# Kernel optimization log

Measured on AMD Instinct MI355X. Metric: run time of the kernel, lower is better.

## Reference

```python
import math
import jax, jax.numpy as jnp
import numpy as np

B, N, L, D, H = 1, 64, 512, 768, 12
DK = D // H


def setup_inputs() -> dict:
    rng = jax.random.key(0)
    ks = jax.random.split(rng, 8)
    s = 0.02  # weight init scale
    return {
        "query": jax.random.normal(ks[0], (B, N, L, D), jnp.float32),
        "key": jax.random.normal(ks[1], (B, N, L, D), jnp.float32),
        "value": jax.random.normal(ks[2], (B, N, L, D), jnp.float32),
        "Wq": jax.random.normal(ks[3], (D, D), jnp.float32) * s,
        "bq": jnp.zeros((D,), jnp.float32),
        "Wk": jax.random.normal(ks[4], (D, D), jnp.float32) * s,
        "bk": jnp.zeros((D,), jnp.float32),
        "Wv": jax.random.normal(ks[5], (D, D), jnp.float32) * s,
        "bv": jnp.zeros((D,), jnp.float32),
        "Wo": jax.random.normal(ks[6], (D, D), jnp.float32) * s,
        "bo": jnp.zeros((D,), jnp.float32),
    }


def reference(query, key, value, Wq, bq, Wk, bk, Wv, bv, Wo, bo):
    b, n, l, d = query.shape
    h, dk = H, DK
    # combined scaling: 1/sqrt(d_k) * 1/sqrt(N)
    scale = 1.0 / (math.sqrt(dk) * math.sqrt(n))
    # nn.Linear: y = x @ W.T + b  (W is [out, in])
    q = (jnp.einsum('bnld,ed->bnle', query, Wq) + bq).reshape(b, n, l, h, dk) * scale
    k = (jnp.einsum('bnld,ed->bnle', key, Wk) + bk).reshape(b, n, l, h, dk)
    v = (jnp.einsum('bnld,ed->bnle', value, Wv) + bv).reshape(b, n, l, h, dk)
    # tied attention: scores summed over the N (sequence-copy) axis BEFORE softmax
    att = jnp.einsum('bnihk,bnjhk->bhij', q, k)  # [B,H,L,L]
    att = jax.nn.softmax(att, axis=-1)  # dropout is identity in eval
    # single attention map broadcast across all N value tensors
    out = jnp.einsum('bhij,bnjhk->bnihk', att, v).reshape(b, n, l, d)
    return jnp.einsum('bnld,ed->bnle', out, Wo) + bo
```

## Files before the change

kernel.cpp:

```cpp
#include <hip/hip_runtime.h>


typedef __bf16 bf16x8 __attribute__((ext_vector_type(8)));
typedef float f32x4 __attribute__((ext_vector_type(4)));

__device__ __forceinline__ unsigned short f2bf(float f) {
  unsigned u = __float_as_uint(f);
  u += 0x7fffu + ((u >> 16) & 1u);
  return (unsigned short)(u >> 16);
}

__device__ __forceinline__ void gll16(const void* g, void* l) {
  __builtin_amdgcn_global_load_lds(
      (const __attribute__((address_space(1))) unsigned int*)g,
      (__attribute__((address_space(3))) unsigned int*)l, 16, 0, 0);
}

#define BAR __builtin_amdgcn_s_barrier()

enum { MODE_QCAT = 0, MODE_VT = 1, MODE_ATT = 2, MODE_OUTWS = 3, MODE_OUT_BIAS = 4 };

template <int MODE>
__global__ __launch_bounds__(512, 2) void gemm256(
    const void* __restrict__ Av, const void* __restrict__ Bv,
    const float* __restrict__ b0, const float* __restrict__ b1,
    void* __restrict__ Cv, int K, int lda, int ldb,
    long long a_bs, long long b_bs, float alpha0, float alpha1,
    long long c_bs, int ntn) {
  __shared__ unsigned short L[2][2][16384];

  const int tid = threadIdx.x;
  const int wave = tid >> 6;
  const int lane = tid & 63;
  const int wm = wave >> 2;
  const int wn = wave & 3;
  const int l15 = lane & 15;
  const int kq8 = lane >> 4;
  const int sw = l15 & 7;

  const int bid = blockIdx.x;
  const int xcd = bid & 7;
  const int kk_ = bid >> 3;
  const int tn = kk_ % ntn;
  const int tm = (kk_ / ntn) * 8 + xcd;
  const int batch = blockIdx.z;

  const long long m0 = (long long)tm * 256;
  const long long n0 = (long long)tn * 256;

  const unsigned short* Ab = (const unsigned short*)Av + (long long)batch * a_bs;
  const unsigned short* Bb = (const unsigned short*)Bv + (long long)batch * b_bs;

  const long long rowAw = m0 + wave * 8 + (lane >> 3);
  const long long rowBw = n0 + wave * 8 + (lane >> 3);
  const int csw = ((lane & 7) ^ (lane >> 3)) << 3;

  f32x4 acc[8][4] = {};

  auto stA = [&](int buf, int q, int k0) {
    gll16(Ab + (rowAw + (q << 6)) * (long long)lda + k0 + csw,
          &L[buf][0][(q << 12) + (wave << 9)]);
  };
  auto stB = [&](int buf, int q, int k0) {
    gll16(Bb + (rowBw + (q << 6)) * (long long)ldb + k0 + csw,
          &L[buf][1][(q << 12) + (wave << 9)]);
  };

  float bpre[4] = {};
  float aa = 1.0f;
  if constexpr (MODE == MODE_QCAT || MODE == MODE_VT || MODE == MODE_OUT_BIAS) {
    const float* bb = batch ? b1 : b0;
    aa = batch ? alpha1 : alpha0;
#pragma unroll
    for (int u = 0; u < 4; ++u) bpre[u] = bb[n0 + wn * 64 + u * 16 + l15];
  }

  const int NT = K >> 6;
#pragma unroll
  for (int q = 0; q < 4; ++q) stB(0, q, 0);
#pragma unroll
  for (int q = 0; q < 4; ++q) stA(0, q, 0);
  if (NT > 1) {
    stA(1, 0, 64);
    stA(1, 2, 64);
    asm volatile("s_waitcnt vmcnt(2)" ::: "memory");
  } else {
    asm volatile("s_waitcnt vmcnt(0)" ::: "memory");
  }
  BAR;

  for (int T = 0; T < NT; ++T) {
    const int cur = T & 1, nxt = cur ^ 1;
    const int k1 = (T + 1) << 6, k2 = (T + 2) << 6;
#pragma unroll
    for (int p = 0; p < 4; ++p) {
      const int kc = p >> 1, mh = p & 1;
      bf16x8 af[4], bfr[4];
#pragma unroll
      for (int mf = 0; mf < 4; ++mf) {
        const int row = wm * 128 + mh * 64 + mf * 16 + l15;
        af[mf] = *(const bf16x8*)&L[cur][0][row * 64 + (((kc << 2) + kq8) ^ sw) * 8];
      }
#pragma unroll
      for (int u = 0; u < 4; ++u) {
        const int row = wn * 64 + u * 16 + l15;
        bfr[u] = *(const bf16x8*)&L[cur][1][row * 64 + (((kc << 2) + kq8) ^ sw) * 8];
      }
      if (p == 0 && T + 1 < NT) { stB(nxt, 0, k1); stB(nxt, 1, k1); }
      if (p == 1 && T + 1 < NT) { stB(nxt, 2, k1); stB(nxt, 3, k1); }
      if (p == 2 && T + 1 < NT) { stA(nxt, 1, k1); stA(nxt, 3, k1); }
      if (p == 3 && T + 2 < NT) { stA(cur, 0, k2); stA(cur, 2, k2); }
      __builtin_amdgcn_s_setprio(1);
#pragma unroll
      for (int mf = 0; mf < 4; ++mf)
#pragma unroll
        for (int u = 0; u < 4; ++u)
          acc[mh * 4 + mf][u] = __builtin_amdgcn_mfma_f32_16x16x32_bf16(
              af[mf], bfr[u], acc[mh * 4 + mf][u], 0, 0, 0);
      __builtin_amdgcn_s_setprio(0);
      if (p == 3) {
        if (T + 1 < NT) {
          if (T + 2 < NT) asm volatile("s_waitcnt vmcnt(2)" ::: "memory");
          else            asm volatile("s_waitcnt vmcnt(0)" ::: "memory");
          BAR;
        }
      } else {
        BAR;
      }
    }
  }

#pragma unroll
  for (int mf = 0; mf < 8; ++mf) {
#pragma unroll
    for (int u = 0; u < 4; ++u) {
      const long long col = n0 + wn * 64 + u * 16 + l15;
#pragma unroll
      for (int r = 0; r < 4; ++r) {
        const long long row = m0 + wm * 128 + mf * 16 + (lane >> 4) * 4 + r;
        float v = acc[mf][u][r];
        if constexpr (MODE == MODE_QCAT) {
          const float vv = (v + bpre[u]) * aa;
          const long long h = col >> 6, kq = col & 63, n = row >> 9, i = row & 511;
          ((unsigned short*)Cv + batch * c_bs)[((h * 512 + i) << 12) + (n << 6) + kq] =
              f2bf(vv);
        } else if constexpr (MODE == MODE_VT) {
          const float vv = v + bpre[u];
          const long long h = col >> 6, kq = col & 63, n = row >> 9, j = row & 511;
          ((unsigned short*)Cv)[(((h << 12) + (n << 6) + kq) << 9) + j] = f2bf(vv);
        } else {
          ((float*)Cv)[row * 768 + col] = v + bpre[u];
        }
      }
    }
  }
}

constexpr int BM = 128, BN = 128, BK = 32;

template <int MODE, bool SWZ, int KS>
__global__ __launch_bounds__(256, 2) void gemm_bt(
    const void* __restrict__ Av, const void* __restrict__ Bv,
    const float* __restrict__ bias, void* __restrict__ Cv,
    int K, int lda, int ldb, long long a_bs, long long b_bs,
    float alpha, int ntn, long long c_bs) {
  constexpr int LP = 32;

  __shared__ unsigned short As0[BM * LP];
  __shared__ unsigned short Bs0[BN * LP];
  __shared__ unsigned short As1[BM * LP];
  __shared__ unsigned short Bs1[BN * LP];

  const int tid = threadIdx.x;
  const int wave = tid >> 6;
  const int lane = tid & 63;
  const int wm = wave >> 1, wn = wave & 1;

  int tm, tn, batch = 0, ks = 0;
  if constexpr (SWZ && MODE == MODE_ATT) {
    const int bid = blockIdx.x;
    const int xcd = bid & 7, j = bid >> 3;
    const int z = (j >> 4) * 8 + xcd;
    const int tile = j & 15;
    tn = tile & 3;
    tm = tile >> 2;
    ks = z % KS;
    batch = z / KS;
  } else if constexpr (SWZ && MODE == MODE_OUTWS) {
    const int bid = blockIdx.x;
    const int xcd = bid & 7, j = bid >> 3;
    const int g = (j >> 6) * 8 + xcd;
    const int idx = j & 63;
    batch = g >> 1;
    tm = idx >> 4;
    tn = (g & 1) * 16 + (idx & 15);
  } else {
    if constexpr (SWZ) {
      const int bid = blockIdx.x;
      const int xcd = bid & 7;
      const int k = bid >> 3;
      tn = k % ntn;
      tm = (k / ntn) * 8 + xcd;
    } else {
      tn = blockIdx.x;
      tm = blockIdx.y;
    }
    batch = blockIdx.z;
    if constexpr (KS > 1) { ks = batch % KS; batch /= KS; }
  }

  const long long m0 = (long long)tm * BM;
  const long long n0 = (long long)tn * BN;

  const unsigned short* Ab = (const unsigned short*)Av + (long long)batch * a_bs + (long long)ks * K;
  const unsigned short* Bb = (const unsigned short*)Bv + (long long)batch * b_bs + (long long)ks * K;

  f32x4 acc[4][4] = {};

  const int l15 = lane & 15;
  const int kq = (lane >> 4) * 8;
  const int r_in = lane >> 2;
  const int c8 = (lane & 3) * 8;

  auto stage = [&](unsigned short* Asb, unsigned short* Bsb, int k0) {
#pragma unroll
    for (int t = 0; t < 2; ++t) {
      const int rb = t * 64 + wave * 16;
      gll16(Ab + (m0 + rb + r_in) * (long long)lda + k0 + c8, &Asb[rb * LP]);
      gll16(Bb + (n0 + rb + r_in) * (long long)ldb + k0 + c8, &Bsb[rb * LP]);
    }
  };
  auto compute = [&](const unsigned short* Asb, const unsigned short* Bsb) {
    bf16x8 af[4], bfr[4];
#pragma unroll
    for (int t = 0; t < 4; ++t)
      af[t] = *(const bf16x8*)&Asb[(wm * 64 + t * 16 + l15) * LP + kq];
#pragma unroll
    for (int u = 0; u < 4; ++u)
      bfr[u] = *(const bf16x8*)&Bsb[(wn * 64 + u * 16 + l15) * LP + kq];
#pragma unroll
    for (int t = 0; t < 4; ++t)
#pragma unroll
      for (int u = 0; u < 4; ++u)
        acc[t][u] = __builtin_amdgcn_mfma_f32_16x16x32_bf16(af[t], bfr[u], acc[t][u], 0, 0, 0);
  };

  stage(As0, Bs0, 0);
  asm volatile("s_waitcnt vmcnt(0)" ::: "memory");
  BAR;

  const int NT = K >> 5;
  for (int t = 0; t < NT; t += 2) {
    stage(As1, Bs1, (t + 1) << 5);
    asm volatile("s_waitcnt vmcnt(4)" ::: "memory");
    BAR;
    compute(As0, Bs0);
    BAR;
    if (t + 2 < NT) {
      stage(As0, Bs0, (t + 2) << 5);
      asm volatile("s_waitcnt vmcnt(4)" ::: "memory");
    } else {
      asm volatile("s_waitcnt vmcnt(0)" ::: "memory");
    }
    BAR;
    compute(As1, Bs1);
    BAR;
  }

#pragma unroll
  for (int t = 0; t < 4; ++t) {
#pragma unroll
    for (int u = 0; u < 4; ++u) {
      const long long col = n0 + wn * 64 + u * 16 + l15;
#pragma unroll
      for (int r = 0; r < 4; ++r) {
        const long long row = m0 + wm * 64 + t * 16 + (lane >> 4) * 4 + r;
        float v = acc[t][u][r];
        if constexpr (MODE == MODE_ATT) {
          float* p = &((float*)Cv)[((long long)batch << 18) + (row << 9) + col];
          if constexpr (KS > 1) atomicAdd(p, v); else *p = v;
        } else if constexpr (MODE == MODE_OUTWS) {
          const long long n = col >> 6, kk = col & 63;
          ((unsigned short*)Cv)[(n * 512 + row) * 768 + (long long)batch * 64 + kk] = f2bf(v);
        } else {
          ((float*)Cv)[row * 768 + col] = v + alpha;
        }
      }
    }
  }
}

__global__ __launch_bounds__(256) void softmax_rows(const float* __restrict__ att,
                                                    unsigned short* __restrict__ outb) {
  const long long rowbase = (long long)blockIdx.x << 9;
  const int tid = threadIdx.x;
  float a = att[rowbase + tid];
  float b = att[rowbase + tid + 256];

  float m = fmaxf(a, b);
#pragma unroll
  for (int off = 32; off; off >>= 1) m = fmaxf(m, __shfl_down(m, off));
  __shared__ float redm[4];
  if ((tid & 63) == 0) redm[tid >> 6] = m;
  __syncthreads();
  m = fmaxf(fmaxf(redm[0], redm[1]), fmaxf(redm[2], redm[3]));

  const float e0 = __expf(a - m), e1 = __expf(b - m);
  float s = e0 + e1;
#pragma unroll
  for (int off = 32; off; off >>= 1) s += __shfl_down(s, off);
  __shared__ float reds[4];
  if ((tid & 63) == 0) reds[tid >> 6] = s;
  __syncthreads();
  s = reds[0] + reds[1] + reds[2] + reds[3];

  const float inv = 1.0f / s;
  outb[rowbase + tid] = f2bf(e0 * inv);
  outb[rowbase + tid + 256] = f2bf(e1 * inv);
}

__global__ __launch_bounds__(256) void cvt_bf16(const float* __restrict__ in,
                                                unsigned short* __restrict__ out) {
  const long long i = ((long long)blockIdx.x * 256 + threadIdx.x) * 8;
  const float4 a = *(const float4*)(in + i);
  const float4 b = *(const float4*)(in + i + 4);
  uint4 p;
  p.x = (unsigned)f2bf(a.x) | ((unsigned)f2bf(a.y) << 16);
  p.y = (unsigned)f2bf(a.z) | ((unsigned)f2bf(a.w) << 16);
  p.z = (unsigned)f2bf(b.x) | ((unsigned)f2bf(b.y) << 16);
  p.w = (unsigned)f2bf(b.z) | ((unsigned)f2bf(b.w) << 16);
  *(uint4*)(out + i) = p;
}

__global__ __launch_bounds__(256) void cvt_qk(
    const float* __restrict__ s0, const float* __restrict__ s1,
    unsigned short* __restrict__ d0, unsigned short* __restrict__ d1) {
  const float* s = blockIdx.y ? s1 : s0;
  unsigned short* d = blockIdx.y ? d1 : d0;
  const long long i = ((long long)blockIdx.x * 256 + threadIdx.x) * 8;
  const float4 a = *(const float4*)(s + i);
  const float4 b = *(const float4*)(s + i + 4);
  uint4 p;
  p.x = (unsigned)f2bf(a.x) | ((unsigned)f2bf(a.y) << 16);
  p.y = (unsigned)f2bf(a.z) | ((unsigned)f2bf(a.w) << 16);
  p.z = (unsigned)f2bf(b.x) | ((unsigned)f2bf(b.y) << 16);
  p.w = (unsigned)f2bf(b.z) | ((unsigned)f2bf(b.w) << 16);
  *(uint4*)(d + i) = p;
}

__global__ __launch_bounds__(256) void cvt_w4(
    const float* __restrict__ s0, const float* __restrict__ s1,
    const float* __restrict__ s2, const float* __restrict__ s3,
    unsigned short* __restrict__ d0, unsigned short* __restrict__ d1,
    unsigned short* __restrict__ d2, unsigned short* __restrict__ d3) {
  const float* s;
  unsigned short* d;
  switch (blockIdx.y) {
    case 0: s = s0; d = d0; break;
    case 1: s = s1; d = d1; break;
    case 2: s = s2; d = d2; break;
    default: s = s3; d = d3; break;
  }
  const long long i = ((long long)blockIdx.x * 256 + threadIdx.x) * 8;
  const float4 a = *(const float4*)(s + i);
  const float4 b = *(const float4*)(s + i + 4);
  uint4 p;
  p.x = (unsigned)f2bf(a.x) | ((unsigned)f2bf(a.y) << 16);
  p.y = (unsigned)f2bf(a.z) | ((unsigned)f2bf(a.w) << 16);
  p.z = (unsigned)f2bf(b.x) | ((unsigned)f2bf(b.y) << 16);
  p.w = (unsigned)f2bf(b.z) | ((unsigned)f2bf(b.w) << 16);
  *(uint4*)(d + i) = p;
}

extern "C" void kernel_launch(void* const* d_in, const int* in_sizes, int n_in,
                              void* d_out, int out_size, void* d_ws, size_t ws_size,
                              hipStream_t stream) {
  const float* query = (const float*)d_in[0];
  const float* key   = (const float*)d_in[1];
  const float* value = (const float*)d_in[2];
  const float* Wq = (const float*)d_in[3];
  const float* bq = (const float*)d_in[4];
  const float* Wk = (const float*)d_in[5];
  const float* bk = (const float*)d_in[6];
  const float* Wv = (const float*)d_in[7];
  const float* bv = (const float*)d_in[8];
  const float* Wo = (const float*)d_in[9];
  const float* bo = (const float*)d_in[10];
  float* out = (float*)d_out;

  char* ws = (char*)d_ws;
  unsigned short* q_ws  = (unsigned short*)(ws);
  unsigned short* k_ws  = (unsigned short*)(ws + 50331648);
  unsigned short* vt_ws = (unsigned short*)(ws + 100663296);
  float*          att   = (float*)(ws + 150994944);
  unsigned short* wo_b  = (unsigned short*)(ws + 163577856);
  unsigned short* wq_b  = (unsigned short*)(ws + 150994944);
  unsigned short* wk_b  = (unsigned short*)(ws + 150994944 + 1179648);
  unsigned short* wv_b  = (unsigned short*)(ws + 150994944 + 2359296);
  unsigned short* att_b = k_ws;
  unsigned short* out_ws = q_ws;
  unsigned short* xb0 = (unsigned short*)d_out;
  unsigned short* xb1 = (unsigned short*)d_out + 25165824;
  (void)wk_b; (void)wv_b;

  const dim3 blk(256);
  const dim3 blk5(512);

  cvt_w4<<<dim3(288, 4), blk, 0, stream>>>(Wo, Wq, Wk, Wv, wo_b, wq_b, wk_b, wv_b);

  cvt_qk<<<dim3(12288, 2), blk, 0, stream>>>(query, key, xb0, xb1);

  gemm256<MODE_QCAT><<<dim3(384, 1, 2), blk5, 0, stream>>>(
      xb0, wq_b, bq, bk, q_ws, 768, 768, 768, 25165824LL, 589824LL,
      0.015625f, 1.0f, 25165824LL, 3);

  cvt_bf16<<<12288, blk, 0, stream>>>(value, xb0);
  gemm256<MODE_VT><<<dim3(384, 1, 1), blk5, 0, stream>>>(
      xb0, wv_b, bv, nullptr, vt_ws, 768, 768, 768, 0, 0, 1.0f, 1.0f, 0, 3);

  hipMemsetAsync(att, 0, 12582912, stream);
  gemm_bt<MODE_ATT, true, 4><<<dim3(768, 1, 1), blk, 0, stream>>>(
      q_ws, k_ws, nullptr, att, 1024, 4096, 4096, 2097152LL, 2097152LL, 1.0f, 0, 0);

  softmax_rows<<<6144, blk, 0, stream>>>(att, att_b);

  gemm_bt<MODE_OUTWS, true, 1><<<dim3(1536, 1, 1), blk, 0, stream>>>(
      att_b, vt_ws, nullptr, out_ws, 512, 512, 512, 262144LL, 2097152LL, 1.0f, 0, 0);

  gemm256<MODE_OUT_BIAS><<<dim3(384, 1, 1), blk5, 0, stream>>>(
      out_ws, wo_b, bo, nullptr, out, 768, 768, 768, 0, 0, 1.0f, 1.0f, 0, 3);
}
```

Measured before the change: 633.3 us.

## Fuse fp32-to-bf16 input conversion into QKV projection GEMM and drop split-K atomics

The separate query/key/value fp32-to-bf16 conversion kernels are removed. The projection GEMM now loads fp32 A tiles into registers, converts them and writes them to LDS, and all three projections run in a single launch with batch index 3. Split-K attention partials are written to separate buffers in the output scratch and summed inside softmax, which replaces the memset and atomicAdd. The cost is a less deep pipeline: prefetch drops from two tiles ahead to one, there is a full vmcnt(0) wait each tile, and A loads go through registers instead of direct global-to-LDS transfers.

```diff
diff --git a/kernel.cpp b/kernel.cpp
--- a/kernel.cpp
+++ b/kernel.cpp
@@ -18,15 +18,16 @@
 
 #define BAR __builtin_amdgcn_s_barrier()
 
-enum { MODE_QCAT = 0, MODE_VT = 1, MODE_ATT = 2, MODE_OUTWS = 3, MODE_OUT_BIAS = 4 };
-
-template <int MODE>
+enum { MODE_PROJ = 0, MODE_ATT = 2, MODE_OUTWS = 3, MODE_OUT_BIAS = 4 };
+
+template <int MODE, bool F32A>
 __global__ __launch_bounds__(512, 2) void gemm256(
-    const void* __restrict__ Av, const void* __restrict__ Bv,
+    const void* __restrict__ A0, const void* __restrict__ A1,
+    const void* __restrict__ A2, const unsigned short* __restrict__ Bw,
     const float* __restrict__ b0, const float* __restrict__ b1,
-    void* __restrict__ Cv, int K, int lda, int ldb,
-    long long a_bs, long long b_bs, float alpha0, float alpha1,
-    long long c_bs, int ntn) {
+    const float* __restrict__ b2, void* __restrict__ Cv,
+    int K, int lda, int ldb, long long b_bs,
+    float alpha0, long long c_bs, int ntn) {
   __shared__ unsigned short L[2][2][16384];
 
   const int tid = threadIdx.x;
@@ -48,16 +49,39 @@
   const long long m0 = (long long)tm * 256;
   const long long n0 = (long long)tn * 256;
 
-  const unsigned short* Ab = (const unsigned short*)Av + (long long)batch * a_bs;
-  const unsigned short* Bb = (const unsigned short*)Bv + (long long)batch * b_bs;
+  const void* Abase;
+  if constexpr (MODE == MODE_PROJ)
+    Abase = batch == 0 ? A0 : (batch == 1 ? A1 : A2);
+  else
+    Abase = A0;
+  const float* Af = (const float*)Abase;
+  const unsigned short* Ab = (const unsigned short*)Abase;
+  const unsigned short* Bb = Bw + (long long)batch * b_bs;
 
   const long long rowAw = m0 + wave * 8 + (lane >> 3);
   const long long rowBw = n0 + wave * 8 + (lane >> 3);
-  const int csw = ((lane & 7) ^ (lane >> 3)) << 3;
+  const int csw = ((lane & 7) ^ (lane >> 3)) * 8;
 
   f32x4 acc[8][4] = {};
-
-  auto stA = [&](int buf, int q, int k0) {
+  f32x4 areg[4][2];
+
+  auto loadA = [&](int k0) {
+#pragma unroll
+    for (int q = 0; q < 4; ++q) {
+      const float* s = Af + (rowAw + (q << 6)) * (long long)lda + k0 + csw;
+      areg[q][0] = *(const f32x4*)s;
+      areg[q][1] = *(const f32x4*)(s + 4);
+    }
+  };
+  auto writeA = [&](int buf, int q) {
+    bf16x8 w;
+    w[0] = (__bf16)areg[q][0][0]; w[1] = (__bf16)areg[q][0][1];
+    w[2] = (__bf16)areg[q][0][2]; w[3] = (__bf16)areg[q][0][3];
+    w[4] = (__bf16)areg[q][1][0]; w[5] = (__bf16)areg[q][1][1];
+    w[6] = (__bf16)areg[q][1][2]; w[7] = (__bf16)areg[q][1][3];
+    *(bf16x8*)&L[buf][0][(q << 12) + (wave << 9) + lane * 8] = w;
+  };
+  auto stA16 = [&](int buf, int q, int k0) {
     gll16(Ab + (rowAw + (q << 6)) * (long long)lda + k0 + csw,
           &L[buf][0][(q << 12) + (wave << 9)]);
   };
@@ -68,30 +92,36 @@
 
   float bpre[4] = {};
   float aa = 1.0f;
-  if constexpr (MODE == MODE_QCAT || MODE == MODE_VT || MODE == MODE_OUT_BIAS) {
-    const float* bb = batch ? b1 : b0;
-    aa = batch ? alpha1 : alpha0;
+  if constexpr (MODE == MODE_PROJ) {
+    const float* bb = batch == 0 ? b0 : (batch == 1 ? b1 : b2);
+    aa = batch == 0 ? alpha0 : 1.0f;
 #pragma unroll
     for (int u = 0; u < 4; ++u) bpre[u] = bb[n0 + wn * 64 + u * 16 + l15];
-  }
+  } else if constexpr (MODE == MODE_OUT_BIAS) {
+#pragma unroll
+    for (int u = 0; u < 4; ++u) bpre[u] = b0[n0 + wn * 64 + u * 16 + l15];
+  }
+
+  if constexpr (F32A) {
+    loadA(0);
+#pragma unroll
+    for (int q = 0; q < 4; ++q) stB(0, q, 0);
+#pragma unroll
+    for (int q = 0; q < 4; ++q) writeA(0, q);
+  } else {
+#pragma unroll
+    for (int q = 0; q < 4; ++q) stA16(0, q, 0);
+#pragma unroll
+    for (int q = 0; q < 4; ++q) stB(0, q, 0);
+  }
+  asm volatile("s_waitcnt vmcnt(0) lgkmcnt(0)" ::: "memory");
+  BAR;
 
   const int NT = K >> 6;
-#pragma unroll
-  for (int q = 0; q < 4; ++q) stB(0, q, 0);
-#pragma unroll
-  for (int q = 0; q < 4; ++q) stA(0, q, 0);
-  if (NT > 1) {
-    stA(1, 0, 64);
-    stA(1, 2, 64);
-    asm volatile("s_waitcnt vmcnt(2)" ::: "memory");
-  } else {
-    asm volatile("s_waitcnt vmcnt(0)" ::: "memory");
-  }
-  BAR;
-
   for (int T = 0; T < NT; ++T) {
     const int cur = T & 1, nxt = cur ^ 1;
-    const int k1 = (T + 1) << 6, k2 = (T + 2) << 6;
+    const int k1 = (T + 1) << 6;
+    const bool more = (T + 1 < NT);
 #pragma unroll
     for (int p = 0; p < 4; ++p) {
       const int kc = p >> 1, mh = p & 1;
@@ -106,10 +136,22 @@
         const int row = wn * 64 + u * 16 + l15;
         bfr[u] = *(const bf16x8*)&L[cur][1][row * 64 + (((kc << 2) + kq8) ^ sw) * 8];
       }
-      if (p == 0 && T + 1 < NT) { stB(nxt, 0, k1); stB(nxt, 1, k1); }
-      if (p == 1 && T + 1 < NT) { stB(nxt, 2, k1); stB(nxt, 3, k1); }
-      if (p == 2 && T + 1 < NT) { stA(nxt, 1, k1); stA(nxt, 3, k1); }
-      if (p == 3 && T + 2 < NT) { stA(cur, 0, k2); stA(cur, 2, k2); }
+      if (p == 0 && more) {
+        if constexpr (F32A) {
+          loadA(k1);
+#pragma unroll
+          for (int q = 0; q < 4; ++q) stB(nxt, q, k1);
+        } else {
+#pragma unroll
+          for (int q = 0; q < 4; ++q) stA16(nxt, q, k1);
+#pragma unroll
+          for (int q = 0; q < 4; ++q) stB(nxt, q, k1);
+        }
+      }
+      if constexpr (F32A) {
+        if (p == 2 && more) { writeA(nxt, 0); writeA(nxt, 1); }
+        if (p == 3 && more) { writeA(nxt, 2); writeA(nxt, 3); }
+      }
       __builtin_amdgcn_s_setprio(1);
 #pragma unroll
       for (int mf = 0; mf < 4; ++mf)
@@ -118,13 +160,10 @@
           acc[mh * 4 + mf][u] = __builtin_amdgcn_mfma_f32_16x16x32_bf16(
               af[mf], bfr[u], acc[mh * 4 + mf][u], 0, 0, 0);
       __builtin_amdgcn_s_setprio(0);
-      if (p == 3) {
-        if (T + 1 < NT) {
-          if (T + 2 < NT) asm volatile("s_waitcnt vmcnt(2)" ::: "memory");
-          else            asm volatile("s_waitcnt vmcnt(0)" ::: "memory");
-          BAR;
-        }
-      } else {
+      if (p < 3) {
+        BAR;
+      } else if (more) {
+        asm volatile("s_waitcnt vmcnt(0) lgkmcnt(0)" ::: "memory");
         BAR;
       }
     }
@@ -139,15 +178,18 @@
       for (int r = 0; r < 4; ++r) {
         const long long row = m0 + wm * 128 + mf * 16 + (lane >> 4) * 4 + r;
         float v = acc[mf][u][r];
-        if constexpr (MODE == MODE_QCAT) {
-          const float vv = (v + bpre[u]) * aa;
-          const long long h = col >> 6, kq = col & 63, n = row >> 9, i = row & 511;
-          ((unsigned short*)Cv + batch * c_bs)[((h * 512 + i) << 12) + (n << 6) + kq] =
-              f2bf(vv);
-        } else if constexpr (MODE == MODE_VT) {
-          const float vv = v + bpre[u];
-          const long long h = col >> 6, kq = col & 63, n = row >> 9, j = row & 511;
-          ((unsigned short*)Cv)[(((h << 12) + (n << 6) + kq) << 9) + j] = f2bf(vv);
+        if constexpr (MODE == MODE_PROJ) {
+          if (batch < 2) {
+            const float vv = (v + bpre[u]) * aa;
+            const long long h = col >> 6, kq = col & 63, n = row >> 9, i = row & 511;
+            ((unsigned short*)Cv + batch * c_bs)[((h * 512 + i) << 12) + (n << 6) + kq] =
+                f2bf(vv);
+          } else {
+            const float vv = v + bpre[u];
+            const long long h = col >> 6, kq = col & 63, n = row >> 9, j = row & 511;
+            ((unsigned short*)Cv + 2 * c_bs)[(((h << 12) + (n << 6) + kq) << 9) + j] =
+                f2bf(vv);
+          }
         } else {
           ((float*)Cv)[row * 768 + col] = v + bpre[u];
         }
@@ -195,16 +237,8 @@
     tm = idx >> 4;
     tn = (g & 1) * 16 + (idx & 15);
   } else {
-    if constexpr (SWZ) {
-      const int bid = blockIdx.x;
-      const int xcd = bid & 7;
-      const int k = bid >> 3;
-      tn = k % ntn;
-      tm = (k / ntn) * 8 + xcd;
-    } else {
-      tn = blockIdx.x;
-      tm = blockIdx.y;
-    }
+    tn = blockIdx.x;
+    tm = blockIdx.y;
     batch = blockIdx.z;
     if constexpr (KS > 1) { ks = batch % KS; batch /= KS; }
   }
@@ -277,8 +311,7 @@
         const long long row = m0 + wm * 64 + t * 16 + (lane >> 4) * 4 + r;
         float v = acc[t][u][r];
         if constexpr (MODE == MODE_ATT) {
-          float* p = &((float*)Cv)[((long long)batch << 18) + (row << 9) + col];
-          if constexpr (KS > 1) atomicAdd(p, v); else *p = v;
+          ((float*)Cv)[((long long)(ks * 12 + batch) << 18) + (row << 9) + col] = v;
         } else if constexpr (MODE == MODE_OUTWS) {
           const long long n = col >> 6, kk = col & 63;
           ((unsigned short*)Cv)[(n * 512 + row) * 768 + (long long)batch * 64 + kk] = f2bf(v);
@@ -294,8 +327,12 @@
                                                     unsigned short* __restrict__ outb) {
   const long long rowbase = (long long)blockIdx.x << 9;
   const int tid = threadIdx.x;
-  float a = att[rowbase + tid];
-  float b = att[rowbase + tid + 256];
+  float a = 0.0f, b = 0.0f;
+#pragma unroll
+  for (int s = 0; s < 4; ++s) {
+    a += att[(long long)s * 3145728 + rowbase + tid];
+    b += att[(long long)s * 3145728 + rowbase + tid + 256];
+  }
 
   float m = fmaxf(a, b);
 #pragma unroll
@@ -317,35 +354,6 @@
   const float inv = 1.0f / s;
   outb[rowbase + tid] = f2bf(e0 * inv);
   outb[rowbase + tid + 256] = f2bf(e1 * inv);
-}
-
-__global__ __launch_bounds__(256) void cvt_bf16(const float* __restrict__ in,
-                                                unsigned short* __restrict__ out) {
-  const long long i = ((long long)blockIdx.x * 256 + threadIdx.x) * 8;
-  const float4 a = *(const float4*)(in + i);
-  const float4 b = *(const float4*)(in + i + 4);
-  uint4 p;
-  p.x = (unsigned)f2bf(a.x) | ((unsigned)f2bf(a.y) << 16);
-  p.y = (unsigned)f2bf(a.z) | ((unsigned)f2bf(a.w) << 16);
-  p.z = (unsigned)f2bf(b.x) | ((unsigned)f2bf(b.y) << 16);
-  p.w = (unsigned)f2bf(b.z) | ((unsigned)f2bf(b.w) << 16);
-  *(uint4*)(out + i) = p;
-}
-
-__global__ __launch_bounds__(256) void cvt_qk(
-    const float* __restrict__ s0, const float* __restrict__ s1,
-    unsigned short* __restrict__ d0, unsigned short* __restrict__ d1) {
-  const float* s = blockIdx.y ? s1 : s0;
-  unsigned short* d = blockIdx.y ? d1 : d0;
-  const long long i = ((long long)blockIdx.x * 256 + threadIdx.x) * 8;
-  const float4 a = *(const float4*)(s + i);
-  const float4 b = *(const float4*)(s + i + 4);
-  uint4 p;
-  p.x = (unsigned)f2bf(a.x) | ((unsigned)f2bf(a.y) << 16);
-  p.y = (unsigned)f2bf(a.z) | ((unsigned)f2bf(a.w) << 16);
-  p.z = (unsigned)f2bf(b.x) | ((unsigned)f2bf(b.y) << 16);
-  p.w = (unsigned)f2bf(b.z) | ((unsigned)f2bf(b.w) << 16);
-  *(uint4*)(d + i) = p;
 }
 
 __global__ __launch_bounds__(256) void cvt_w4(
@@ -392,41 +400,34 @@
   unsigned short* q_ws  = (unsigned short*)(ws);
   unsigned short* k_ws  = (unsigned short*)(ws + 50331648);
   unsigned short* vt_ws = (unsigned short*)(ws + 100663296);
-  float*          att   = (float*)(ws + 150994944);
-  unsigned short* wo_b  = (unsigned short*)(ws + 163577856);
   unsigned short* wq_b  = (unsigned short*)(ws + 150994944);
   unsigned short* wk_b  = (unsigned short*)(ws + 150994944 + 1179648);
   unsigned short* wv_b  = (unsigned short*)(ws + 150994944 + 2359296);
+  unsigned short* wo_b  = (unsigned short*)(ws + 150994944 + 3538944);
   unsigned short* att_b = k_ws;
   unsigned short* out_ws = q_ws;
-  unsigned short* xb0 = (unsigned short*)d_out;
-  unsigned short* xb1 = (unsigned short*)d_out + 25165824;
-  (void)wk_b; (void)wv_b;
+  float* att_part = (float*)d_out;
 
   const dim3 blk(256);
   const dim3 blk5(512);
 
-  cvt_w4<<<dim3(288, 4), blk, 0, stream>>>(Wo, Wq, Wk, Wv, wo_b, wq_b, wk_b, wv_b);
-
-  cvt_qk<<<dim3(12288, 2), blk, 0, stream>>>(query, key, xb0, xb1);
-
-  gemm256<MODE_QCAT><<<dim3(384, 1, 2), blk5, 0, stream>>>(
-      xb0, wq_b, bq, bk, q_ws, 768, 768, 768, 25165824LL, 589824LL,
-      0.015625f, 1.0f, 25165824LL, 3);
-
-  cvt_bf16<<<12288, blk, 0, stream>>>(value, xb0);
-  gemm256<MODE_VT><<<dim3(384, 1, 1), blk5, 0, stream>>>(
-      xb0, wv_b, bv, nullptr, vt_ws, 768, 768, 768, 0, 0, 1.0f, 1.0f, 0, 3);
-
-  hipMemsetAsync(att, 0, 12582912, stream);
+  cvt_w4<<<dim3(288, 4), blk, 0, stream>>>(Wq, Wk, Wv, Wo, wq_b, wk_b, wv_b, wo_b);
+
+  gemm256<MODE_PROJ, true><<<dim3(384, 1, 3), blk5, 0, stream>>>(
+      query, key, value, wq_b, bq, bk, bv, q_ws,
+      768, 768, 768, 589824LL, 0.015625f, 25165824LL, 3);
+
   gemm_bt<MODE_ATT, true, 4><<<dim3(768, 1, 1), blk, 0, stream>>>(
-      q_ws, k_ws, nullptr, att, 1024, 4096, 4096, 2097152LL, 2097152LL, 1.0f, 0, 0);
-
-  softmax_rows<<<6144, blk, 0, stream>>>(att, att_b);
+      q_ws, k_ws, nullptr, att_part, 1024, 4096, 4096, 2097152LL, 2097152LL,
+      1.0f, 0, 0);
+
+  softmax_rows<<<6144, blk, 0, stream>>>(att_part, att_b);
 
   gemm_bt<MODE_OUTWS, true, 1><<<dim3(1536, 1, 1), blk, 0, stream>>>(
-      att_b, vt_ws, nullptr, out_ws, 512, 512, 512, 262144LL, 2097152LL, 1.0f, 0, 0);
-
-  gemm256<MODE_OUT_BIAS><<<dim3(384, 1, 1), blk5, 0, stream>>>(
-      out_ws, wo_b, bo, nullptr, out, 768, 768, 768, 0, 0, 1.0f, 1.0f, 0, 3);
-}
+      att_b, vt_ws, nullptr, out_ws, 512, 512, 512, 262144LL, 2097152LL,
+      1.0f, 0, 0);
+
+  gemm256<MODE_OUT_BIAS, false><<<dim3(384, 1, 1), blk5, 0, stream>>>(
+      out_ws, nullptr, nullptr, wo_b, bo, nullptr, nullptr, out,
+      768, 768, 768, 0, 1.0f, 0, 3);
+}
```

After: 659.5 us. 1.04x slower.
